# Optimization experiments

Hardware: AMD Instinct MI355X
Metric: run time of the kernel (lower is better)

## Reference

```python
import jax, jax.numpy as jnp
import numpy as np

N, E, NF, EF = 2048, 65536, 128, 64
HID, NH, HD, FF, L = 256, 8, 32, 1024, 4
OUT, MAXN = 1280, 4096


def setup_inputs() -> dict:
    key = jax.random.key(0)
    ks = iter(jax.random.split(key, 64))
    def rn(shape, s=0.02):
        return jax.random.normal(next(ks), shape, jnp.float32) * s
    inp = dict(
        node_features=jax.random.normal(next(ks), (N, NF), jnp.float32),
        edge_features=jax.random.normal(next(ks), (E, EF), jnp.float32),
        edge_index=jax.random.randint(next(ks), (2, E), 0, N),
        W_node=rn((NF, HID)), b_node=jnp.zeros((HID,)),
        W_edge=rn((EF, HID)), b_edge=jnp.zeros((HID,)),
        pos_emb=rn((MAXN, HID), 1.0),
        Wq=rn((L, HID, HID)), bq=jnp.zeros((L, HID)),
        Wk=rn((L, HID, HID)), bk=jnp.zeros((L, HID)),
        Wv=rn((L, HID, HID)), bv=jnp.zeros((L, HID)),
        Wo=rn((L, HID, HID)), bo=jnp.zeros((L, HID)),
        Wep=rn((L, HID, NH)), bep=jnp.zeros((L, NH)),
        Wf1=rn((L, HID, FF)), bf1=jnp.zeros((L, FF)),
        Wf2=rn((L, FF, HID)), bf2=jnp.zeros((L, HID)),
        g1=jnp.ones((L, HID)), be1=jnp.zeros((L, HID)),
        g2=jnp.ones((L, HID)), be2=jnp.zeros((L, HID)),
        g_ln=jnp.ones((HID,)), b_ln=jnp.zeros((HID,)),
        Wp1=rn((HID, HID)), bp1=jnp.zeros((HID,)),
        Wp2=rn((HID, 1)), bp2=jnp.zeros((1,)),
        Wo1=rn((3 * HID, 2 * HID)), bo1=jnp.zeros((2 * HID,)),
        Wo2=rn((2 * HID, OUT)), bo2=jnp.zeros((OUT,)),
    )
    return inp


def _ln(x, g, b, eps=1e-5):
    m = x.mean(-1, keepdims=True)
    v = ((x - m) ** 2).mean(-1, keepdims=True)
    return (x - m) * jax.lax.rsqrt(v + eps) * g + b


def reference(node_features, edge_features, edge_index, W_node, b_node, W_edge,
              b_edge, pos_emb, Wq, bq, Wk, bk, Wv, bv, Wo, bo, Wep, bep,
              Wf1, bf1, Wf2, bf2, g1, be1, g2, be2, g_ln, b_ln,
              Wp1, bp1, Wp2, bp2, Wo1, bo1, Wo2, bo2):
    n = node_features.shape[0]
    src, dst = edge_index[0], edge_index[1]
    scale = float(np.sqrt(HD))
    # node encoding + learned positional embedding (n <= max_nodes path)
    x = node_features @ W_node + b_node + pos_emb[:n]
    edge_attr = edge_features @ W_edge + b_edge  # [E, HID]
    # symmetric adjacency mask with self-loops
    adj = jnp.zeros((n, n), bool).at[src, dst].set(True).at[dst, src].set(True)
    adj = adj.at[jnp.arange(n), jnp.arange(n)].set(True)
    for i in range(L):
        Q = (x @ Wq[i] + bq[i]).reshape(n, NH, HD)
        K = (x @ Wk[i] + bk[i]).reshape(n, NH, HD)
        V = (x @ Wv[i] + bv[i]).reshape(n, NH, HD)
        scores = jnp.einsum('nhd,mhd->nmh', Q, K) / scale  # [n, n, NH]
        ebias = edge_attr @ Wep[i] + bep[i]  # [E, NH]
        scores = scores.at[src, dst].add(ebias)  # accumulating scatter, same as per-edge loop
        scores = jnp.where(adj[:, None, :], scores.transpose(0, 2, 1), -jnp.inf)  # [n, NH, n]
        attn = jax.nn.softmax(scores, axis=-1)
        ctx = jnp.einsum('nhm,mhd->nhd', attn, V).reshape(n, HID)
        a = ctx @ Wo[i] + bo[i]
        x = _ln(x + a, g1[i], be1[i])
        f = jax.nn.gelu(x @ Wf1[i] + bf1[i], approximate=False) @ Wf2[i] + bf2[i]
        x = _ln(x + f, g2[i], be2[i])
    x = _ln(x, g_ln, b_ln)
    # global pooling (batch=None path): mean / max / attention
    mean_p = x.mean(0, keepdims=True)
    max_p = x.max(0, keepdims=True)
    aw = jax.nn.softmax(jnp.tanh(x @ Wp1 + bp1) @ Wp2 + bp2, axis=0)  # [n, 1]
    attn_p = (x * aw).sum(0, keepdims=True)
    g = jnp.concatenate([mean_p, max_p, attn_p], axis=1)  # [1, 3*HID]
    out = jax.nn.relu(g @ Wo1 + bo1) @ Wo2 + bo2  # [1, OUT]
    return out
```

## Files before the change

### kernel.cpp

```cpp
#include <hip/hip_runtime.h>
#include <math.h>

#define NNODE 2048
#define NEDGE 65536
#define HIDN  256
#define NHEAD 8
#define HDIM  32
#define FFD   1024
#define NLAYER 4
#define OUTD  1280
#define NNZ_MAX (2*NEDGE + NNODE)

typedef __attribute__((ext_vector_type(8))) short bf16x8;
typedef __attribute__((ext_vector_type(4))) float f32x4;

__device__ __forceinline__ unsigned short f2b(float f) {
    unsigned u = __float_as_uint(f);
    unsigned r = (u + 0x7fffu + ((u >> 16) & 1u)) >> 16;
    return (unsigned short)r;
}
__device__ __forceinline__ float b2f(unsigned short u) {
    return __uint_as_float((unsigned)u << 16);
}

template<int EPI, int OUT>
__global__ __launch_bounds__(256)
void mgemm(const unsigned short* __restrict__ A, const unsigned short* __restrict__ Bt,
           const float* __restrict__ bias, const float* __restrict__ extra,
           float* __restrict__ Cf, unsigned short* __restrict__ Cb,
           int M, int N, int K)
{
    __shared__ __align__(16) unsigned short As[64 * 40];
    __shared__ __align__(16) unsigned short Bs[64 * 40];
    int tid = threadIdx.x;
    int bm0 = blockIdx.y * 64, bn0 = blockIdx.x * 64;
    int wave = tid >> 6, lane = tid & 63;
    int wm = (wave >> 1) * 32, wn = (wave & 1) * 32;
    int srow = tid >> 2, skoff = (tid & 3) * 8;
    int lrow = lane & 15, quad = lane >> 4;
    f32x4 acc[2][2] = {};
    for (int k0 = 0; k0 < K; k0 += 32) {
        *(uint4*)(&As[srow*40 + skoff]) = *(const uint4*)(A  + (size_t)(bm0+srow)*K + k0 + skoff);
        *(uint4*)(&Bs[srow*40 + skoff]) = *(const uint4*)(Bt + (size_t)(bn0+srow)*K + k0 + skoff);
        __syncthreads();
        bf16x8 af[2], bfr[2];
        #pragma unroll
        for (int i = 0; i < 2; i++) af[i]  = *(const bf16x8*)(&As[(wm + i*16 + lrow)*40 + quad*8]);
        #pragma unroll
        for (int j = 0; j < 2; j++) bfr[j] = *(const bf16x8*)(&Bs[(wn + j*16 + lrow)*40 + quad*8]);
        #pragma unroll
        for (int i = 0; i < 2; i++)
            #pragma unroll
            for (int j = 0; j < 2; j++)
                acc[i][j] = __builtin_amdgcn_mfma_f32_16x16x32_bf16(af[i], bfr[j], acc[i][j], 0, 0, 0);
        __syncthreads();
    }
    #pragma unroll
    for (int i = 0; i < 2; i++)
        #pragma unroll
        for (int j = 0; j < 2; j++) {
            int col = bn0 + wn + j*16 + lrow;
            float bv = bias[col];
            #pragma unroll
            for (int r = 0; r < 4; r++) {
                int row = bm0 + wm + i*16 + quad*4 + r;
                float v = acc[i][j][r] + bv;
                if (EPI == 1) v = 0.5f * v * (1.f + erff(v * 0.70710678118654752f));
                else if (EPI == 2) v = tanhf(v);
                else if (EPI == 3) v += extra[(size_t)row*N + col];
                if (OUT == 0 || OUT == 2) Cf[(size_t)row*N + col] = v;
                if (OUT == 1 || OUT == 2) Cb[(size_t)row*N + col] = f2b(v);
            }
        }
}

__global__ __launch_bounds__(256)
void transpose_bf16(const float* __restrict__ src, unsigned short* __restrict__ dst,
                    int K, int N, long srcStride, long dstStride)
{
    __shared__ unsigned short tile[32][33];
    const float* s = src + (size_t)blockIdx.z * srcStride;
    unsigned short* d = dst + (size_t)blockIdx.z * dstStride;
    int n0 = blockIdx.x * 32, k0 = blockIdx.y * 32;
    int tx = threadIdx.x & 31, ty = threadIdx.x >> 5;
    #pragma unroll
    for (int i = 0; i < 4; i++)
        tile[ty + i*8][tx] = f2b(s[(size_t)(k0 + ty + i*8) * N + n0 + tx]);
    __syncthreads();
    #pragma unroll
    for (int i = 0; i < 4; i++)
        d[(size_t)(n0 + ty + i*8) * K + k0 + tx] = tile[tx][ty + i*8];
}

__global__ void conv_bf16(const float* __restrict__ s, unsigned short* __restrict__ d, int n)
{
    int t = blockIdx.x * 256 + threadIdx.x;
    if (t < n) d[t] = f2b(s[t]);
}

__global__ void concat_qkv_bias(const float* __restrict__ bq, const float* __restrict__ bk,
                                const float* __restrict__ bv, float* __restrict__ bqkv)
{
    int t = blockIdx.x * 256 + threadIdx.x;
    if (t >= NLAYER * 768) return;
    int l = t / 768, j = t % 768;
    float v = (j < 256) ? bq[l*256 + j] : (j < 512 ? bk[l*256 + j - 256] : bv[l*256 + j - 512]);
    bqkv[t] = v;
}

__global__ void adj_build(const int* __restrict__ src, const int* __restrict__ dst,
                          unsigned* __restrict__ adjbits)
{
    int t = blockIdx.x * blockDim.x + threadIdx.x;
    if (t < NEDGE) {
        int s = src[t], d = dst[t];
        atomicOr(&adjbits[(size_t)s*64 + (d >> 5)], 1u << (d & 31));
        atomicOr(&adjbits[(size_t)d*64 + (s >> 5)], 1u << (s & 31));
    }
    if (t < NNODE)
        atomicOr(&adjbits[(size_t)t*64 + (t >> 5)], 1u << (t & 31));
}

__global__ void row_rank(const unsigned* __restrict__ adjbits,
                         unsigned* __restrict__ rowcum, int* __restrict__ deg)
{
    int i = blockIdx.x * blockDim.x + threadIdx.x;
    if (i >= NNODE) return;
    unsigned c = 0;
    for (int w = 0; w < 64; w++) {
        rowcum[i*64 + w] = c;
        c += __popc(adjbits[i*64 + w]);
    }
    deg[i] = (int)c;
}

__global__ __launch_bounds__(256)
void scan_kernel(const int* __restrict__ deg, int* __restrict__ rowoff)
{
    __shared__ int part[256];
    int tid = threadIdx.x;
    int base = tid * 8;
    int local[8]; int s = 0;
    #pragma unroll
    for (int k = 0; k < 8; k++) { local[k] = s; s += deg[base + k]; }
    part[tid] = s;
    __syncthreads();
    for (int off = 1; off < 256; off <<= 1) {
        int v = (tid >= off) ? part[tid - off] : 0;
        __syncthreads();
        part[tid] += v;
        __syncthreads();
    }
    int pre = (tid == 0) ? 0 : part[tid - 1];
    #pragma unroll
    for (int k = 0; k < 8; k++) rowoff[base + k] = pre + local[k];
    if (tid == 255) rowoff[NNODE] = part[255];
}

__global__ void fill_cols(const unsigned* __restrict__ adjbits,
                          const int* __restrict__ rowoff, int* __restrict__ cols)
{
    int i = blockIdx.x * blockDim.x + threadIdx.x;
    if (i >= NNODE) return;
    int base = rowoff[i];
    for (int w = 0; w < 64; w++) {
        unsigned bits = adjbits[i*64 + w];
        while (bits) {
            int b = __ffs(bits) - 1;
            cols[base++] = w*32 + b;
            bits &= bits - 1;
        }
    }
}

__global__ void wcomb_kernel(const float* __restrict__ W_edge, const float* __restrict__ b_edge,
                             const float* __restrict__ Wep, const float* __restrict__ bep,
                             float* __restrict__ Wcomb, float* __restrict__ bcomb)
{
    int t = blockIdx.x * blockDim.x + threadIdx.x;
    if (t < 64*32) {
        int k = t >> 5, lh = t & 31, l = lh >> 3, h = lh & 7;
        float acc = 0.f;
        for (int c = 0; c < HIDN; c++)
            acc += W_edge[k*HIDN + c] * Wep[l*HIDN*NHEAD + c*NHEAD + h];
        Wcomb[k*32 + lh] = acc;
    } else if (t < 64*32 + 32) {
        int lh = t - 64*32, l = lh >> 3, h = lh & 7;
        float acc = bep[l*NHEAD + h];
        for (int c = 0; c < HIDN; c++)
            acc += b_edge[c] * Wep[l*HIDN*NHEAD + c*NHEAD + h];
        bcomb[lh] = acc;
    }
}

__global__ __launch_bounds__(256)
void ebias_kernel(const float* __restrict__ ef, const float* __restrict__ Wcomb,
                  const float* __restrict__ bcomb, float* __restrict__ out)
{
    __shared__ float Wl[64*32];
    __shared__ float bl[32];
    int tid = threadIdx.x;
    for (int k = tid; k < 64*32; k += 256) Wl[k] = Wcomb[k];
    if (tid < 32) bl[tid] = bcomb[tid];
    __syncthreads();
    int t = blockIdx.x * 256 + tid;
    int e = t >> 5, lh = t & 31;
    const float* f = ef + (size_t)e * 64;
    float acc = bl[lh];
    #pragma unroll
    for (int k = 0; k < 64; k++) acc += f[k] * Wl[k*32 + lh];
    out[(size_t)e*32 + lh] = acc;
}

__global__ void scatter_bias(const int* __restrict__ src, const int* __restrict__ dst,
                             const unsigned* __restrict__ adjbits,
                             const unsigned* __restrict__ rowcum,
                             const int* __restrict__ rowoff,
                             const float* __restrict__ ebias, float* __restrict__ bias_csr)
{
    int t = blockIdx.x * blockDim.x + threadIdx.x;
    int e = t >> 5;
    if (e >= NEDGE) return;
    int lh = t & 31;
    int s = src[e], d = dst[e];
    unsigned wbits = adjbits[(size_t)s*64 + (d >> 5)];
    int rank = (int)rowcum[(size_t)s*64 + (d >> 5)] + __popc(wbits & ((1u << (d & 31)) - 1u));
    int slot = rowoff[s] + rank;
    atomicAdd(&bias_csr[(size_t)slot*32 + lh], ebias[(size_t)e*32 + lh]);
}

__global__ __launch_bounds__(256)
void attn_kernel(const unsigned short* __restrict__ QKVb, const int* __restrict__ rowoff,
                 const int* __restrict__ cols, const float* __restrict__ bias_csr,
                 unsigned short* __restrict__ ctxb, int layer)
{
    __shared__ float mS[4][8], lS[4][8];
    __shared__ __align__(16) float accS[4][256];
    int i = blockIdx.x;
    int tid = threadIdx.x;
    int w = tid >> 6, lane = tid & 63;
    int h = lane >> 3;
    int off = lane * 4;
    ushort4 qu = *(const ushort4*)(QKVb + (size_t)i*768 + off);
    float4 qf = { b2f(qu.x), b2f(qu.y), b2f(qu.z), b2f(qu.w) };
    int start = rowoff[i], end = rowoff[i+1];
    int lh0 = layer * 8 + h;
    float m = -INFINITY, l = 0.f;
    float4 acc = {0.f, 0.f, 0.f, 0.f};
    for (int c0 = start + w; c0 < end; c0 += 256) {
        int myslot = c0 + 4*lane;
        int mycol = (myslot < end) ? cols[myslot] : 0;
        int lim = min(end, c0 + 256);
        int it = 0;
        for (int slot = c0; slot < lim; slot += 4, ++it) {
            int j = __shfl(mycol, it);
            ushort4 ku = *(const ushort4*)(QKVb + (size_t)j*768 + 256 + off);
            float s = qf.x*b2f(ku.x) + qf.y*b2f(ku.y) + qf.z*b2f(ku.z) + qf.w*b2f(ku.w);
            s += __shfl_xor(s, 1);
            s += __shfl_xor(s, 2);
            s += __shfl_xor(s, 4);
            s = s * 0.17677669529663687f + bias_csr[(size_t)slot*32 + lh0];
            float mn = fmaxf(m, s);
            float sc = __expf(m - mn);
            float p  = __expf(s - mn);
            ushort4 vu = *(const ushort4*)(QKVb + (size_t)j*768 + 512 + off);
            acc.x = acc.x*sc + p*b2f(vu.x);
            acc.y = acc.y*sc + p*b2f(vu.y);
            acc.z = acc.z*sc + p*b2f(vu.z);
            acc.w = acc.w*sc + p*b2f(vu.w);
            l = l*sc + p;
            m = mn;
        }
    }
    if ((lane & 7) == 0) { mS[w][h] = m; lS[w][h] = l; }
    *(float4*)&accS[w][off] = acc;
    __syncthreads();
    if (w == 0) {
        float m0 = mS[0][h], m1 = mS[1][h], m2 = mS[2][h], m3 = mS[3][h];
        float mx = fmaxf(fmaxf(m0, m1), fmaxf(m2, m3));
        float e0 = (m0 == -INFINITY) ? 0.f : __expf(m0 - mx);
        float e1 = (m1 == -INFINITY) ? 0.f : __expf(m1 - mx);
        float e2 = (m2 == -INFINITY) ? 0.f : __expf(m2 - mx);
        float e3 = (m3 == -INFINITY) ? 0.f : __expf(m3 - mx);
        float ls = lS[0][h]*e0 + lS[1][h]*e1 + lS[2][h]*e2 + lS[3][h]*e3;
        float4 a0 = *(float4*)&accS[0][off];
        float4 a1 = *(float4*)&accS[1][off];
        float4 a2 = *(float4*)&accS[2][off];
        float4 a3 = *(float4*)&accS[3][off];
        float inv = 1.f / ls;
        ushort4 o;
        o.x = f2b((a0.x*e0 + a1.x*e1 + a2.x*e2 + a3.x*e3) * inv);
        o.y = f2b((a0.y*e0 + a1.y*e1 + a2.y*e2 + a3.y*e3) * inv);
        o.z = f2b((a0.z*e0 + a1.z*e1 + a2.z*e2 + a3.z*e3) * inv);
        o.w = f2b((a0.w*e0 + a1.w*e1 + a2.w*e2 + a3.w*e3) * inv);
        *(ushort4*)(ctxb + (size_t)i*HIDN + off) = o;
    }
}

template<bool RES>
__global__ __launch_bounds__(256)
void ln_kernel(float* __restrict__ x, const float* __restrict__ r,
               const float* __restrict__ g, const float* __restrict__ b,
               unsigned short* __restrict__ xb)
{
    __shared__ float lds[4];
    int row = blockIdx.x, c = threadIdx.x;
    float v = x[(size_t)row*HIDN + c];
    if (RES) v += r[(size_t)row*HIDN + c];
    float s = v;
    for (int mm = 1; mm < 64; mm <<= 1) s += __shfl_xor(s, mm);
    if ((c & 63) == 0) lds[c >> 6] = s;
    __syncthreads();
    float mean = (lds[0] + lds[1] + lds[2] + lds[3]) * (1.f / HIDN);
    __syncthreads();
    float dv = v - mean;
    float qq = dv * dv;
    for (int mm = 1; mm < 64; mm <<= 1) qq += __shfl_xor(qq, mm);
    if ((c & 63) == 0) lds[c >> 6] = qq;
    __syncthreads();
    float var = (lds[0] + lds[1] + lds[2] + lds[3]) * (1.f / HIDN);
    float rs = rsqrtf(var + 1e-5f);
    float o = dv * rs * g[c] + b[c];
    x[(size_t)row*HIDN + c] = o;
    xb[(size_t)row*HIDN + c] = f2b(o);
}

__global__ void pool_score(const float* __restrict__ t, const float* __restrict__ Wp2,
                           const float* __restrict__ bp2, float* __restrict__ s)
{
    int i = blockIdx.x * blockDim.x + threadIdx.x;
    if (i >= NNODE) return;
    float acc = bp2[0];
    for (int c = 0; c < HIDN; c++) acc += t[(size_t)i*HIDN + c] * Wp2[c];
    s[i] = acc;
}

__global__ __launch_bounds__(1024)
void softmax_nodes(const float* __restrict__ s, float* __restrict__ aw)
{
    __shared__ float lds[16];
    __shared__ float red;
    int tid = threadIdx.x;
    float a = s[tid], b = s[tid + 1024];
    float mx = fmaxf(a, b);
    for (int mm = 1; mm < 64; mm <<= 1) mx = fmaxf(mx, __shfl_xor(mx, mm));
    if ((tid & 63) == 0) lds[tid >> 6] = mx;
    __syncthreads();
    if (tid == 0) { float v = -INFINITY; for (int k = 0; k < 16; k++) v = fmaxf(v, lds[k]); red = v; }
    __syncthreads();
    mx = red;
    float ea = __expf(a - mx), eb = __expf(b - mx);
    float ss = ea + eb;
    for (int mm = 1; mm < 64; mm <<= 1) ss += __shfl_xor(ss, mm);
    __syncthreads();
    if ((tid & 63) == 0) lds[tid >> 6] = ss;
    __syncthreads();
    if (tid == 0) { float v = 0.f; for (int k = 0; k < 16; k++) v += lds[k]; red = v; }
    __syncthreads();
    ss = red;
    aw[tid] = ea / ss;
    aw[tid + 1024] = eb / ss;
}

__global__ __launch_bounds__(256)
void pool_kernel(const float* __restrict__ x, const float* __restrict__ aw,
                 float* __restrict__ g)
{
    __shared__ float l1[4], l2[4], l3[4];
    int c = blockIdx.x, tid = threadIdx.x;
    float sm = 0.f, mx = -INFINITY, ap = 0.f;
    for (int r = tid; r < NNODE; r += 256) {
        float v = x[(size_t)r*HIDN + c];
        sm += v;
        mx = fmaxf(mx, v);
        ap += v * aw[r];
    }
    for (int mm = 1; mm < 64; mm <<= 1) {
        sm += __shfl_xor(sm, mm);
        mx = fmaxf(mx, __shfl_xor(mx, mm));
        ap += __shfl_xor(ap, mm);
    }
    if ((tid & 63) == 0) { int w = tid >> 6; l1[w] = sm; l2[w] = mx; l3[w] = ap; }
    __syncthreads();
    if (tid == 0) {
        sm = l1[0] + l1[1] + l1[2] + l1[3];
        mx = fmaxf(fmaxf(l2[0], l2[1]), fmaxf(l2[2], l2[3]));
        ap = l3[0] + l3[1] + l3[2] + l3[3];
        g[c]          = sm * (1.f / NNODE);
        g[HIDN + c]   = mx;
        g[2*HIDN + c] = ap;
    }
}

__global__ __launch_bounds__(512)
void head1(const float* __restrict__ g, const float* __restrict__ Wo1,
           const float* __restrict__ bo1, float* __restrict__ h1)
{
    __shared__ float gs[3*HIDN];
    int tid = threadIdx.x;
    for (int k = tid; k < 3*HIDN; k += 512) gs[k] = g[k];
    __syncthreads();
    float acc = bo1[tid];
    for (int k = 0; k < 3*HIDN; k++) acc += gs[k] * Wo1[(size_t)k*512 + tid];
    h1[tid] = fmaxf(acc, 0.f);
}

__global__ __launch_bounds__(256)
void head2(const float* __restrict__ h1, const float* __restrict__ Wo2,
           const float* __restrict__ bo2, float* __restrict__ out)
{
    __shared__ float hs[512];
    int tid = threadIdx.x;
    int j = blockIdx.x * 256 + tid;
    for (int k = tid; k < 512; k += 256) hs[k] = h1[k];
    __syncthreads();
    float acc = bo2[j];
    for (int k = 0; k < 512; k++) acc += hs[k] * Wo2[(size_t)k*OUTD + j];
    out[j] = acc;
}

extern "C" void kernel_launch(void* const* d_in, const int* in_sizes, int n_in,
                              void* d_out, int out_size, void* d_ws, size_t ws_size,
                              hipStream_t stream)
{
    const float* node_features = (const float*)d_in[0];
    const float* edge_features = (const float*)d_in[1];
    const int*   edge_index    = (const int*)d_in[2];
    const float* W_node = (const float*)d_in[3];
    const float* b_node = (const float*)d_in[4];
    const float* W_edge = (const float*)d_in[5];
    const float* b_edge = (const float*)d_in[6];
    const float* pos_emb = (const float*)d_in[7];
    const float* Wq = (const float*)d_in[8];
    const float* bq = (const float*)d_in[9];
    const float* Wk = (const float*)d_in[10];
    const float* bk = (const float*)d_in[11];
    const float* Wv = (const float*)d_in[12];
    const float* bv = (const float*)d_in[13];
    const float* Wo = (const float*)d_in[14];
    const float* bo = (const float*)d_in[15];
    const float* Wep = (const float*)d_in[16];
    const float* bep = (const float*)d_in[17];
    const float* Wf1 = (const float*)d_in[18];
    const float* bf1 = (const float*)d_in[19];
    const float* Wf2 = (const float*)d_in[20];
    const float* bf2 = (const float*)d_in[21];
    const float* g1  = (const float*)d_in[22];
    const float* be1 = (const float*)d_in[23];
    const float* g2  = (const float*)d_in[24];
    const float* be2 = (const float*)d_in[25];
    const float* g_ln = (const float*)d_in[26];
    const float* b_ln = (const float*)d_in[27];
    const float* Wp1 = (const float*)d_in[28];
    const float* bp1 = (const float*)d_in[29];
    const float* Wp2 = (const float*)d_in[30];
    const float* bp2 = (const float*)d_in[31];
    const float* Wo1 = (const float*)d_in[32];
    const float* bo1 = (const float*)d_in[33];
    const float* Wo2 = (const float*)d_in[34];
    const float* bo2 = (const float*)d_in[35];
    const int* src = edge_index;
    const int* dst = edge_index + NEDGE;

    char* w = (char*)d_ws;
    auto carve = [&](size_t nbytes) {
        void* p = (void*)w;
        w += (nbytes + 255) & ~(size_t)255;
        return p;
    };
    float* x        = (float*)carve((size_t)NNODE*HIDN*4);
    unsigned short* xb = (unsigned short*)carve((size_t)NNODE*HIDN*2);
    unsigned short* bufQKVb = (unsigned short*)carve((size_t)NNODE*768*2);
    float* bufO     = (float*)carve((size_t)NNODE*HIDN*4);
    float* bufP     = (float*)carve((size_t)NNODE*HIDN*4);
    unsigned short* bufAb = (unsigned short*)carve((size_t)NNODE*HIDN*2);
    void*  scratchA = carve((size_t)NEDGE*32*4);
    float* bufE     = (float*)scratchA;
    unsigned short* bufFb = (unsigned short*)scratchA;
    float* Wcomb    = (float*)carve(64*32*4);
    float* bcomb    = (float*)carve(32*4);
    unsigned* adjbits = (unsigned*)carve((size_t)NNODE*64*4);
    unsigned* rowcum  = (unsigned*)carve((size_t)NNODE*64*4);
    int* deg    = (int*)carve(NNODE*4);
    int* rowoff = (int*)carve((NNODE+1)*4);
    int* colsb  = (int*)carve((size_t)NNZ_MAX*4);
    float* bias_csr = (float*)carve((size_t)NNZ_MAX*32*4);
    float* sbuf  = (float*)carve(NNODE*4);
    float* awbuf = (float*)carve(NNODE*4);
    float* gbuf  = (float*)carve(3*HIDN*4);
    float* h1buf = (float*)carve(512*4);
    unsigned short* nf_b  = (unsigned short*)carve((size_t)NNODE*128*2);
    unsigned short* WnT   = (unsigned short*)carve((size_t)HIDN*128*2);
    unsigned short* WqkvT = (unsigned short*)carve((size_t)NLAYER*768*HIDN*2);
    float*          bqkv  = (float*)carve((size_t)NLAYER*768*4);
    unsigned short* WoT   = (unsigned short*)carve((size_t)NLAYER*HIDN*HIDN*2);
    unsigned short* Wf1T  = (unsigned short*)carve((size_t)NLAYER*FFD*HIDN*2);
    unsigned short* Wf2T  = (unsigned short*)carve((size_t)NLAYER*HIDN*FFD*2);
    unsigned short* Wp1T  = (unsigned short*)carve((size_t)HIDN*HIDN*2);

    hipMemsetAsync(adjbits, 0, (size_t)NNODE*64*4, stream);
    hipMemsetAsync(bias_csr, 0, (size_t)NNZ_MAX*32*4, stream);
    adj_build<<<(NEDGE+255)/256, 256, 0, stream>>>(src, dst, adjbits);
    row_rank<<<NNODE/256, 256, 0, stream>>>(adjbits, rowcum, deg);
    scan_kernel<<<1, 256, 0, stream>>>(deg, rowoff);
    fill_cols<<<NNODE/256, 256, 0, stream>>>(adjbits, rowoff, colsb);
    wcomb_kernel<<<(64*32+32+255)/256, 256, 0, stream>>>(W_edge, b_edge, Wep, bep, Wcomb, bcomb);
    ebias_kernel<<<(NEDGE*32)/256, 256, 0, stream>>>(edge_features, Wcomb, bcomb, bufE);
    scatter_bias<<<(NEDGE*32)/256, 256, 0, stream>>>(src, dst, adjbits, rowcum, rowoff, bufE, bias_csr);

    conv_bf16<<<(NNODE*128)/256, 256, 0, stream>>>(node_features, nf_b, NNODE*128);
    transpose_bf16<<<dim3(HIDN/32, 128/32, 1), 256, 0, stream>>>(W_node, WnT, 128, HIDN, 0, 0);
    transpose_bf16<<<dim3(8, 8, NLAYER), 256, 0, stream>>>(Wq, WqkvT,            HIDN, HIDN, 65536, 196608);
    transpose_bf16<<<dim3(8, 8, NLAYER), 256, 0, stream>>>(Wk, WqkvT + 65536,    HIDN, HIDN, 65536, 196608);
    transpose_bf16<<<dim3(8, 8, NLAYER), 256, 0, stream>>>(Wv, WqkvT + 131072,   HIDN, HIDN, 65536, 196608);
    transpose_bf16<<<dim3(8, 8, NLAYER), 256, 0, stream>>>(Wo, WoT, HIDN, HIDN, 65536, 65536);
    transpose_bf16<<<dim3(FFD/32, HIDN/32, NLAYER), 256, 0, stream>>>(Wf1, Wf1T, HIDN, FFD, 262144, 262144);
    transpose_bf16<<<dim3(HIDN/32, FFD/32, NLAYER), 256, 0, stream>>>(Wf2, Wf2T, FFD, HIDN, 262144, 262144);
    transpose_bf16<<<dim3(8, 8, 1), 256, 0, stream>>>(Wp1, Wp1T, HIDN, HIDN, 0, 0);
    concat_qkv_bias<<<(NLAYER*768+255)/256, 256, 0, stream>>>(bq, bk, bv, bqkv);

    mgemm<3,2><<<dim3(HIDN/64, NNODE/64), 256, 0, stream>>>(nf_b, WnT, b_node, pos_emb, x, xb, NNODE, HIDN, 128);

    for (int l = 0; l < NLAYER; l++) {
        mgemm<0,1><<<dim3(768/64, NNODE/64), 256, 0, stream>>>(
            xb, WqkvT + (size_t)l*768*HIDN, bqkv + l*768, nullptr, nullptr, bufQKVb, NNODE, 768, HIDN);
        attn_kernel<<<NNODE, 256, 0, stream>>>(bufQKVb, rowoff, colsb, bias_csr, bufAb, l);
        mgemm<0,0><<<dim3(HIDN/64, NNODE/64), 256, 0, stream>>>(
            bufAb, WoT + (size_t)l*HIDN*HIDN, bo + l*HIDN, nullptr, bufO, nullptr, NNODE, HIDN, HIDN);
        ln_kernel<true><<<NNODE, 256, 0, stream>>>(x, bufO, g1 + l*HIDN, be1 + l*HIDN, xb);
        mgemm<1,1><<<dim3(FFD/64, NNODE/64), 256, 0, stream>>>(
            xb, Wf1T + (size_t)l*FFD*HIDN, bf1 + l*FFD, nullptr, nullptr, bufFb, NNODE, FFD, HIDN);
        mgemm<0,0><<<dim3(HIDN/64, NNODE/64), 256, 0, stream>>>(
            bufFb, Wf2T + (size_t)l*HIDN*FFD, bf2 + l*HIDN, nullptr, bufO, nullptr, NNODE, HIDN, FFD);
        ln_kernel<true><<<NNODE, 256, 0, stream>>>(x, bufO, g2 + l*HIDN, be2 + l*HIDN, xb);
    }

    ln_kernel<false><<<NNODE, 256, 0, stream>>>(x, nullptr, g_ln, b_ln, xb);
    mgemm<2,0><<<dim3(HIDN/64, NNODE/64), 256, 0, stream>>>(xb, Wp1T, bp1, nullptr, bufP, nullptr, NNODE, HIDN, HIDN);
    pool_score<<<NNODE/256, 256, 0, stream>>>(bufP, Wp2, bp2, sbuf);
    softmax_nodes<<<1, 1024, 0, stream>>>(sbuf, awbuf);
    pool_kernel<<<HIDN, 256, 0, stream>>>(x, awbuf, gbuf);
    head1<<<1, 512, 0, stream>>>(gbuf, Wo1, bo1, h1buf);
    head2<<<OUTD/256, 256, 0, stream>>>(h1buf, Wo2, bo2, (float*)d_out);
}
```

Measured before the change: 554.9 us.

## Fuse preprocessing and pooling kernels, prefetch GEMM tiles, parallelize CSR column fill

The GEMM now takes K as a template parameter and loads the next K-chunk from global memory into registers while the current tile is in LDS. All weight transposes are merged into one launch, and so are the conversion and bias concat, the edge-bias compute and scatter, and the pooling score, softmax and head kernels. The pooling score uses an atomic row reduction inside the GEMM epilogue and drops bp2, which is valid because softmax is shift-invariant. fill_cols now runs one thread per 32-bit word instead of one per row. Together these remove launch overhead and intermediate buffers, at the cost of atomics, some redundant exp work per pool block and a larger FFN buffer.

```diff
diff --git a/kernel.cpp b/kernel.cpp
--- a/kernel.cpp
+++ b/kernel.cpp
@@ -23,12 +23,12 @@
     return __uint_as_float((unsigned)u << 16);
 }
 
-template<int EPI, int OUT>
+template<int K, int EPI, int OUT>
 __global__ __launch_bounds__(256)
 void mgemm(const unsigned short* __restrict__ A, const unsigned short* __restrict__ Bt,
            const float* __restrict__ bias, const float* __restrict__ extra,
            float* __restrict__ Cf, unsigned short* __restrict__ Cb,
-           int M, int N, int K)
+           int M, int N, const float* __restrict__ Wp2, float* __restrict__ sred)
 {
     __shared__ __align__(16) unsigned short As[64 * 40];
     __shared__ __align__(16) unsigned short Bs[64 * 40];
@@ -38,11 +38,21 @@
     int wm = (wave >> 1) * 32, wn = (wave & 1) * 32;
     int srow = tid >> 2, skoff = (tid & 3) * 8;
     int lrow = lane & 15, quad = lane >> 4;
+    const unsigned short* ap = A  + (size_t)(bm0 + srow) * K + skoff;
+    const unsigned short* bp = Bt + (size_t)(bn0 + srow) * K + skoff;
+    uint4 av = *(const uint4*)ap;
+    uint4 bv = *(const uint4*)bp;
     f32x4 acc[2][2] = {};
-    for (int k0 = 0; k0 < K; k0 += 32) {
-        *(uint4*)(&As[srow*40 + skoff]) = *(const uint4*)(A  + (size_t)(bm0+srow)*K + k0 + skoff);
-        *(uint4*)(&Bs[srow*40 + skoff]) = *(const uint4*)(Bt + (size_t)(bn0+srow)*K + k0 + skoff);
+    constexpr int NC = K / 32;
+    #pragma unroll 8
+    for (int c = 0; c < NC; ++c) {
+        *(uint4*)(&As[srow*40 + skoff]) = av;
+        *(uint4*)(&Bs[srow*40 + skoff]) = bv;
         __syncthreads();
+        if (c + 1 < NC) {
+            av = *(const uint4*)(ap + (c+1)*32);
+            bv = *(const uint4*)(bp + (c+1)*32);
+        }
         bf16x8 af[2], bfr[2];
         #pragma unroll
         for (int i = 0; i < 2; i++) af[i]  = *(const bf16x8*)(&As[(wm + i*16 + lrow)*40 + quad*8]);
@@ -55,16 +65,38 @@
                 acc[i][j] = __builtin_amdgcn_mfma_f32_16x16x32_bf16(af[i], bfr[j], acc[i][j], 0, 0, 0);
         __syncthreads();
     }
+    if (EPI == 4) {
+        #pragma unroll
+        for (int i = 0; i < 2; i++) {
+            #pragma unroll
+            for (int r = 0; r < 4; r++) {
+                int row = bm0 + wm + i*16 + quad*4 + r;
+                float ps = 0.f;
+                #pragma unroll
+                for (int j = 0; j < 2; j++) {
+                    int col = bn0 + wn + j*16 + lrow;
+                    float v = tanhf(acc[i][j][r] + bias[col]);
+                    ps += v * Wp2[col];
+                }
+                ps += __shfl_xor(ps, 1);
+                ps += __shfl_xor(ps, 2);
+                ps += __shfl_xor(ps, 4);
+                ps += __shfl_xor(ps, 8);
+                if (lrow == 0) atomicAdd(&sred[row], ps);
+            }
+        }
+        return;
+    }
     #pragma unroll
     for (int i = 0; i < 2; i++)
         #pragma unroll
         for (int j = 0; j < 2; j++) {
             int col = bn0 + wn + j*16 + lrow;
-            float bv = bias[col];
+            float bvv = bias[col];
             #pragma unroll
             for (int r = 0; r < 4; r++) {
                 int row = bm0 + wm + i*16 + quad*4 + r;
-                float v = acc[i][j][r] + bv;
+                float v = acc[i][j][r] + bvv;
                 if (EPI == 1) v = 0.5f * v * (1.f + erff(v * 0.70710678118654752f));
                 else if (EPI == 2) v = tanhf(v);
                 else if (EPI == 3) v += extra[(size_t)row*N + col];
@@ -75,13 +107,41 @@
 }
 
 __global__ __launch_bounds__(256)
-void transpose_bf16(const float* __restrict__ src, unsigned short* __restrict__ dst,
-                    int K, int N, long srcStride, long dstStride)
+void transpose_all(const float* __restrict__ Wq, const float* __restrict__ Wk,
+                   const float* __restrict__ Wv, const float* __restrict__ Wo,
+                   const float* __restrict__ Wf1, const float* __restrict__ Wf2,
+                   const float* __restrict__ W_node, const float* __restrict__ Wp1,
+                   unsigned short* __restrict__ WqkvT, unsigned short* __restrict__ WoT,
+                   unsigned short* __restrict__ Wf1T, unsigned short* __restrict__ Wf2T,
+                   unsigned short* __restrict__ WnT, unsigned short* __restrict__ Wp1T)
 {
     __shared__ unsigned short tile[32][33];
-    const float* s = src + (size_t)blockIdx.z * srcStride;
-    unsigned short* d = dst + (size_t)blockIdx.z * dstStride;
-    int n0 = blockIdx.x * 32, k0 = blockIdx.y * 32;
+    int bid = blockIdx.x;
+    const float* s; unsigned short* d; int K, N, n0, k0;
+    if (bid < 1024) {
+        int mat = bid >> 6, rem = bid & 63;
+        int m4 = mat & 3, l = mat >> 2;
+        s = (m4 == 0 ? Wq : m4 == 1 ? Wk : m4 == 2 ? Wv : Wo) + (size_t)l * 65536;
+        d = (m4 < 3) ? WqkvT + (size_t)l*196608 + (size_t)m4*65536
+                     : WoT + (size_t)l*65536;
+        K = 256; N = 256; n0 = (rem & 7) * 32; k0 = (rem >> 3) * 32;
+    } else if (bid < 2048) {
+        int idx = bid - 1024; int l = idx >> 8, rem = idx & 255;
+        s = Wf1 + (size_t)l*262144; d = Wf1T + (size_t)l*262144;
+        K = 256; N = 1024; n0 = (rem & 31) * 32; k0 = (rem >> 5) * 32;
+    } else if (bid < 3072) {
+        int idx = bid - 2048; int l = idx >> 8, rem = idx & 255;
+        s = Wf2 + (size_t)l*262144; d = Wf2T + (size_t)l*262144;
+        K = 1024; N = 256; n0 = (rem & 7) * 32; k0 = (rem >> 3) * 32;
+    } else if (bid < 3104) {
+        int rem = bid - 3072;
+        s = W_node; d = WnT;
+        K = 128; N = 256; n0 = (rem & 7) * 32; k0 = (rem >> 3) * 32;
+    } else {
+        int rem = bid - 3104;
+        s = Wp1; d = Wp1T;
+        K = 256; N = 256; n0 = (rem & 7) * 32; k0 = (rem >> 3) * 32;
+    }
     int tx = threadIdx.x & 31, ty = threadIdx.x >> 5;
     #pragma unroll
     for (int i = 0; i < 4; i++)
@@ -92,20 +152,21 @@
         d[(size_t)(n0 + ty + i*8) * K + k0 + tx] = tile[tx][ty + i*8];
 }
 
-__global__ void conv_bf16(const float* __restrict__ s, unsigned short* __restrict__ d, int n)
+__global__ void misc_prep(const float* __restrict__ nf, unsigned short* __restrict__ nf_b,
+                          const float* __restrict__ bq, const float* __restrict__ bk,
+                          const float* __restrict__ bv, float* __restrict__ bqkv)
 {
     int t = blockIdx.x * 256 + threadIdx.x;
-    if (t < n) d[t] = f2b(s[t]);
-}
-
-__global__ void concat_qkv_bias(const float* __restrict__ bq, const float* __restrict__ bk,
-                                const float* __restrict__ bv, float* __restrict__ bqkv)
-{
-    int t = blockIdx.x * 256 + threadIdx.x;
-    if (t >= NLAYER * 768) return;
-    int l = t / 768, j = t % 768;
-    float v = (j < 256) ? bq[l*256 + j] : (j < 512 ? bk[l*256 + j - 256] : bv[l*256 + j - 512]);
-    bqkv[t] = v;
+    if (t < NNODE*128) {
+        nf_b[t] = f2b(nf[t]);
+    } else {
+        int u = t - NNODE*128;
+        if (u < NLAYER*768) {
+            int l = u / 768, j = u % 768;
+            float v = (j < 256) ? bq[l*256 + j] : (j < 512 ? bk[l*256 + j - 256] : bv[l*256 + j - 512]);
+            bqkv[u] = v;
+        }
+    }
 }
 
 __global__ void adj_build(const int* __restrict__ src, const int* __restrict__ dst,
@@ -157,19 +218,18 @@
     if (tid == 255) rowoff[NNODE] = part[255];
 }
 
-__global__ void fill_cols(const unsigned* __restrict__ adjbits,
-                          const int* __restrict__ rowoff, int* __restrict__ cols)
-{
-    int i = blockIdx.x * blockDim.x + threadIdx.x;
-    if (i >= NNODE) return;
-    int base = rowoff[i];
-    for (int w = 0; w < 64; w++) {
-        unsigned bits = adjbits[i*64 + w];
-        while (bits) {
-            int b = __ffs(bits) - 1;
-            cols[base++] = w*32 + b;
-            bits &= bits - 1;
-        }
+__global__ __launch_bounds__(256)
+void fill_cols(const unsigned* __restrict__ adjbits, const int* __restrict__ rowoff,
+               const unsigned* __restrict__ rowcum, int* __restrict__ cols)
+{
+    int t = blockIdx.x * 256 + threadIdx.x;
+    int i = t >> 6, w = t & 63;
+    unsigned bits = adjbits[(size_t)i*64 + w];
+    int base = rowoff[i] + (int)rowcum[(size_t)i*64 + w];
+    while (bits) {
+        int b = __ffs(bits) - 1;
+        cols[base++] = w*32 + b;
+        bits &= bits - 1;
     }
 }
 
@@ -194,8 +254,12 @@
 }
 
 __global__ __launch_bounds__(256)
-void ebias_kernel(const float* __restrict__ ef, const float* __restrict__ Wcomb,
-                  const float* __restrict__ bcomb, float* __restrict__ out)
+void edge_bias_scatter(const float* __restrict__ ef, const float* __restrict__ Wcomb,
+                       const float* __restrict__ bcomb,
+                       const int* __restrict__ src, const int* __restrict__ dst,
+                       const unsigned* __restrict__ adjbits,
+                       const unsigned* __restrict__ rowcum,
+                       const int* __restrict__ rowoff, float* __restrict__ bias_csr)
 {
     __shared__ float Wl[64*32];
     __shared__ float bl[32];
@@ -209,24 +273,11 @@
     float acc = bl[lh];
     #pragma unroll
     for (int k = 0; k < 64; k++) acc += f[k] * Wl[k*32 + lh];
-    out[(size_t)e*32 + lh] = acc;
-}
-
-__global__ void scatter_bias(const int* __restrict__ src, const int* __restrict__ dst,
-                             const unsigned* __restrict__ adjbits,
-                             const unsigned* __restrict__ rowcum,
-                             const int* __restrict__ rowoff,
-                             const float* __restrict__ ebias, float* __restrict__ bias_csr)
-{
-    int t = blockIdx.x * blockDim.x + threadIdx.x;
-    int e = t >> 5;
-    if (e >= NEDGE) return;
-    int lh = t & 31;
     int s = src[e], d = dst[e];
     unsigned wbits = adjbits[(size_t)s*64 + (d >> 5)];
     int rank = (int)rowcum[(size_t)s*64 + (d >> 5)] + __popc(wbits & ((1u << (d & 31)) - 1u));
     int slot = rowoff[s] + rank;
-    atomicAdd(&bias_csr[(size_t)slot*32 + lh], ebias[(size_t)e*32 + lh]);
+    atomicAdd(&bias_csr[(size_t)slot*32 + lh], acc);
 }
 
 __global__ __launch_bounds__(256)
@@ -325,55 +376,38 @@
     xb[(size_t)row*HIDN + c] = f2b(o);
 }
 
-__global__ void pool_score(const float* __restrict__ t, const float* __restrict__ Wp2,
-                           const float* __restrict__ bp2, float* __restrict__ s)
-{
-    int i = blockIdx.x * blockDim.x + threadIdx.x;
-    if (i >= NNODE) return;
-    float acc = bp2[0];
-    for (int c = 0; c < HIDN; c++) acc += t[(size_t)i*HIDN + c] * Wp2[c];
-    s[i] = acc;
-}
-
-__global__ __launch_bounds__(1024)
-void softmax_nodes(const float* __restrict__ s, float* __restrict__ aw)
-{
-    __shared__ float lds[16];
-    __shared__ float red;
-    int tid = threadIdx.x;
-    float a = s[tid], b = s[tid + 1024];
-    float mx = fmaxf(a, b);
-    for (int mm = 1; mm < 64; mm <<= 1) mx = fmaxf(mx, __shfl_xor(mx, mm));
-    if ((tid & 63) == 0) lds[tid >> 6] = mx;
-    __syncthreads();
-    if (tid == 0) { float v = -INFINITY; for (int k = 0; k < 16; k++) v = fmaxf(v, lds[k]); red = v; }
-    __syncthreads();
-    mx = red;
-    float ea = __expf(a - mx), eb = __expf(b - mx);
-    float ss = ea + eb;
-    for (int mm = 1; mm < 64; mm <<= 1) ss += __shfl_xor(ss, mm);
-    __syncthreads();
-    if ((tid & 63) == 0) lds[tid >> 6] = ss;
-    __syncthreads();
-    if (tid == 0) { float v = 0.f; for (int k = 0; k < 16; k++) v += lds[k]; red = v; }
-    __syncthreads();
-    ss = red;
-    aw[tid] = ea / ss;
-    aw[tid + 1024] = eb / ss;
-}
-
-__global__ __launch_bounds__(256)
-void pool_kernel(const float* __restrict__ x, const float* __restrict__ aw,
-                 float* __restrict__ g)
-{
+__global__ __launch_bounds__(256)
+void pool_fused(const float* __restrict__ x, const float* __restrict__ sred,
+                float* __restrict__ g)
+{
+    __shared__ float sl[NNODE];
+    __shared__ float red[4];
     __shared__ float l1[4], l2[4], l3[4];
     int c = blockIdx.x, tid = threadIdx.x;
+    float mxs = -INFINITY;
+    for (int r = tid; r < NNODE; r += 256) {
+        float v = sred[r];
+        sl[r] = v;
+        mxs = fmaxf(mxs, v);
+    }
+    for (int mm = 1; mm < 64; mm <<= 1) mxs = fmaxf(mxs, __shfl_xor(mxs, mm));
+    if ((tid & 63) == 0) red[tid >> 6] = mxs;
+    __syncthreads();
+    mxs = fmaxf(fmaxf(red[0], red[1]), fmaxf(red[2], red[3]));
+    __syncthreads();
+    float ss = 0.f;
+    for (int r = tid; r < NNODE; r += 256) ss += __expf(sl[r] - mxs);
+    for (int mm = 1; mm < 64; mm <<= 1) ss += __shfl_xor(ss, mm);
+    if ((tid & 63) == 0) red[tid >> 6] = ss;
+    __syncthreads();
+    ss = red[0] + red[1] + red[2] + red[3];
+    float inv = 1.f / ss;
     float sm = 0.f, mx = -INFINITY, ap = 0.f;
     for (int r = tid; r < NNODE; r += 256) {
         float v = x[(size_t)r*HIDN + c];
         sm += v;
         mx = fmaxf(mx, v);
-        ap += v * aw[r];
+        ap += v * __expf(sl[r] - mxs) * inv;
     }
     for (int mm = 1; mm < 64; mm <<= 1) {
         sm += __shfl_xor(sm, mm);
@@ -393,30 +427,24 @@
 }
 
 __global__ __launch_bounds__(512)
-void head1(const float* __restrict__ g, const float* __restrict__ Wo1,
-           const float* __restrict__ bo1, float* __restrict__ h1)
+void head_fused(const float* __restrict__ g, const float* __restrict__ Wo1,
+                const float* __restrict__ bo1, const float* __restrict__ Wo2,
+                const float* __restrict__ bo2, float* __restrict__ out)
 {
     __shared__ float gs[3*HIDN];
+    __shared__ float hs[512];
     int tid = threadIdx.x;
     for (int k = tid; k < 3*HIDN; k += 512) gs[k] = g[k];
     __syncthreads();
     float acc = bo1[tid];
     for (int k = 0; k < 3*HIDN; k++) acc += gs[k] * Wo1[(size_t)k*512 + tid];
-    h1[tid] = fmaxf(acc, 0.f);
-}
-
-__global__ __launch_bounds__(256)
-void head2(const float* __restrict__ h1, const float* __restrict__ Wo2,
-           const float* __restrict__ bo2, float* __restrict__ out)
-{
-    __shared__ float hs[512];
-    int tid = threadIdx.x;
-    int j = blockIdx.x * 256 + tid;
-    for (int k = tid; k < 512; k += 256) hs[k] = h1[k];
-    __syncthreads();
-    float acc = bo2[j];
-    for (int k = 0; k < 512; k++) acc += hs[k] * Wo2[(size_t)k*OUTD + j];
-    out[j] = acc;
+    hs[tid] = fmaxf(acc, 0.f);
+    __syncthreads();
+    for (int j = tid; j < OUTD; j += 512) {
+        float a2 = bo2[j];
+        for (int k = 0; k < 512; k++) a2 += hs[k] * Wo2[(size_t)k*OUTD + j];
+        out[j] = a2;
+    }
 }
 
 extern "C" void kernel_launch(void* const* d_in, const int* in_sizes, int n_in,
@@ -459,6 +487,7 @@
     const float* bo1 = (const float*)d_in[33];
     const float* Wo2 = (const float*)d_in[34];
     const float* bo2 = (const float*)d_in[35];
+    (void)bp2;
     const int* src = edge_index;
     const int* dst = edge_index + NEDGE;
 
@@ -472,23 +501,18 @@
     unsigned short* xb = (unsigned short*)carve((size_t)NNODE*HIDN*2);
     unsigned short* bufQKVb = (unsigned short*)carve((size_t)NNODE*768*2);
     float* bufO     = (float*)carve((size_t)NNODE*HIDN*4);
-    float* bufP     = (float*)carve((size_t)NNODE*HIDN*4);
     unsigned short* bufAb = (unsigned short*)carve((size_t)NNODE*HIDN*2);
-    void*  scratchA = carve((size_t)NEDGE*32*4);
-    float* bufE     = (float*)scratchA;
-    unsigned short* bufFb = (unsigned short*)scratchA;
+    unsigned short* bufFb = (unsigned short*)carve((size_t)NNODE*FFD*2);
     float* Wcomb    = (float*)carve(64*32*4);
     float* bcomb    = (float*)carve(32*4);
     unsigned* adjbits = (unsigned*)carve((size_t)NNODE*64*4);
+    float* bias_csr = (float*)carve((size_t)NNZ_MAX*32*4);
+    float* sbuf  = (float*)carve(NNODE*4);
     unsigned* rowcum  = (unsigned*)carve((size_t)NNODE*64*4);
     int* deg    = (int*)carve(NNODE*4);
     int* rowoff = (int*)carve((NNODE+1)*4);
     int* colsb  = (int*)carve((size_t)NNZ_MAX*4);
-    float* bias_csr = (float*)carve((size_t)NNZ_MAX*32*4);
-    float* sbuf  = (float*)carve(NNODE*4);
-    float* awbuf = (float*)carve(NNODE*4);
     float* gbuf  = (float*)carve(3*HIDN*4);
-    float* h1buf = (float*)carve(512*4);
     unsigned short* nf_b  = (unsigned short*)carve((size_t)NNODE*128*2);
     unsigned short* WnT   = (unsigned short*)carve((size_t)HIDN*128*2);
     unsigned short* WqkvT = (unsigned short*)carve((size_t)NLAYER*768*HIDN*2);
@@ -498,48 +522,41 @@
     unsigned short* Wf2T  = (unsigned short*)carve((size_t)NLAYER*HIDN*FFD*2);
     unsigned short* Wp1T  = (unsigned short*)carve((size_t)HIDN*HIDN*2);
 
-    hipMemsetAsync(adjbits, 0, (size_t)NNODE*64*4, stream);
-    hipMemsetAsync(bias_csr, 0, (size_t)NNZ_MAX*32*4, stream);
+    hipMemsetAsync(adjbits, 0,
+                   (size_t)NNODE*64*4 + (size_t)NNZ_MAX*32*4 + (size_t)NNODE*4, stream);
     adj_build<<<(NEDGE+255)/256, 256, 0, stream>>>(src, dst, adjbits);
     row_rank<<<NNODE/256, 256, 0, stream>>>(adjbits, rowcum, deg);
     scan_kernel<<<1, 256, 0, stream>>>(deg, rowoff);
-    fill_cols<<<NNODE/256, 256, 0, stream>>>(adjbits, rowoff, colsb);
+    fill_cols<<<(NNODE*64)/256, 256, 0, stream>>>(adjbits, rowoff, rowcum, colsb);
     wcomb_kernel<<<(64*32+32+255)/256, 256, 0, stream>>>(W_edge, b_edge, Wep, bep, Wcomb, bcomb);
-    ebias_kernel<<<(NEDGE*32)/256, 256, 0, stream>>>(edge_features, Wcomb, bcomb, bufE);
-    scatter_bias<<<(NEDGE*32)/256, 256, 0, stream>>>(src, dst, adjbits, rowcum, rowoff, bufE, bias_csr);
-
-    conv_bf16<<<(NNODE*128)/256, 256, 0, stream>>>(node_features, nf_b, NNODE*128);
-    transpose_bf16<<<dim3(HIDN/32, 128/32, 1), 256, 0, stream>>>(W_node, WnT, 128, HIDN, 0, 0);
-    transpose_bf16<<<dim3(8, 8, NLAYER), 256, 0, stream>>>(Wq, WqkvT,            HIDN, HIDN, 65536, 196608);
-    transpose_bf16<<<dim3(8, 8, NLAYER), 256, 0, stream>>>(Wk, WqkvT + 65536,    HIDN, HIDN, 65536, 196608);
-    transpose_bf16<<<dim3(8, 8, NLAYER), 256, 0, stream>>>(Wv, WqkvT + 131072,   HIDN, HIDN, 65536, 196608);
-    transpose_bf16<<<dim3(8, 8, NLAYER), 256, 0, stream>>>(Wo, WoT, HIDN, HIDN, 65536, 65536);
-    transpose_bf16<<<dim3(FFD/32, HIDN/32, NLAYER), 256, 0, stream>>>(Wf1, Wf1T, HIDN, FFD, 262144, 262144);
-    transpose_bf16<<<dim3(HIDN/32, FFD/32, NLAYER), 256, 0, stream>>>(Wf2, Wf2T, FFD, HIDN, 262144, 262144);
-    transpose_bf16<<<dim3(8, 8, 1), 256, 0, stream>>>(Wp1, Wp1T, HIDN, HIDN, 0, 0);
-    concat_qkv_bias<<<(NLAYER*768+255)/256, 256, 0, stream>>>(bq, bk, bv, bqkv);
-
-    mgemm<3,2><<<dim3(HIDN/64, NNODE/64), 256, 0, stream>>>(nf_b, WnT, b_node, pos_emb, x, xb, NNODE, HIDN, 128);
+    edge_bias_scatter<<<(NEDGE*32)/256, 256, 0, stream>>>(
+        edge_features, Wcomb, bcomb, src, dst, adjbits, rowcum, rowoff, bias_csr);
+
+    misc_prep<<<(NNODE*128 + NLAYER*768 + 255)/256, 256, 0, stream>>>(
+        node_features, nf_b, bq, bk, bv, bqkv);
+    transpose_all<<<3168, 256, 0, stream>>>(Wq, Wk, Wv, Wo, Wf1, Wf2, W_node, Wp1,
+                                            WqkvT, WoT, Wf1T, Wf2T, WnT, Wp1T);
+
+    mgemm<128,3,2><<<dim3(HIDN/64, NNODE/64), 256, 0, stream>>>(
+        nf_b, WnT, b_node, pos_emb, x, xb, NNODE, HIDN, nullptr, nullptr);
 
     for (int l = 0; l < NLAYER; l++) {
-        mgemm<0,1><<<dim3(768/64, NNODE/64), 256, 0, stream>>>(
-            xb, WqkvT + (size_t)l*768*HIDN, bqkv + l*768, nullptr, nullptr, bufQKVb, NNODE, 768, HIDN);
+        mgemm<256,0,1><<<dim3(768/64, NNODE/64), 256, 0, stream>>>(
+            xb, WqkvT + (size_t)l*768*HIDN, bqkv + l*768, nullptr, nullptr, bufQKVb, NNODE, 768, nullptr, nullptr);
         attn_kernel<<<NNODE, 256, 0, stream>>>(bufQKVb, rowoff, colsb, bias_csr, bufAb, l);
-        mgemm<0,0><<<dim3(HIDN/64, NNODE/64), 256, 0, stream>>>(
-            bufAb, WoT + (size_t)l*HIDN*HIDN, bo + l*HIDN, nullptr, bufO, nullptr, NNODE, HIDN, HIDN);
+        mgemm<256,0,0><<<dim3(HIDN/64, NNODE/64), 256, 0, stream>>>(
+            bufAb, WoT + (size_t)l*HIDN*HIDN, bo + l*HIDN, nullptr, bufO, nullptr, NNODE, HIDN, nullptr, nullptr);
         ln_kernel<true><<<NNODE, 256, 0, stream>>>(x, bufO, g1 + l*HIDN, be1 + l*HIDN, xb);
-        mgemm<1,1><<<dim3(FFD/64, NNODE/64), 256, 0, stream>>>(
-            xb, Wf1T + (size_t)l*FFD*HIDN, bf1 + l*FFD, nullptr, nullptr, bufFb, NNODE, FFD, HIDN);
-        mgemm<0,0><<<dim3(HIDN/64, NNODE/64), 256, 0, stream>>>(
-            bufFb, Wf2T + (size_t)l*HIDN*FFD, bf2 + l*HIDN, nullptr, bufO, nullptr, NNODE, HIDN, FFD);
+        mgemm<256,1,1><<<dim3(FFD/64, NNODE/64), 256, 0, stream>>>(
+            xb, Wf1T + (size_t)l*FFD*HIDN, bf1 + l*FFD, nullptr, nullptr, bufFb, NNODE, FFD, nullptr, nullptr);
+        mgemm<1024,0,0><<<dim3(HIDN/64, NNODE/64), 256, 0, stream>>>(
+            bufFb, Wf2T + (size_t)l*HIDN*FFD, bf2 + l*HIDN, nullptr, bufO, nullptr, NNODE, HIDN, nullptr, nullptr);
         ln_kernel<true><<<NNODE, 256, 0, stream>>>(x, bufO, g2 + l*HIDN, be2 + l*HIDN, xb);
     }
 
     ln_kernel<false><<<NNODE, 256, 0, stream>>>(x, nullptr, g_ln, b_ln, xb);
-    mgemm<2,0><<<dim3(HIDN/64, NNODE/64), 256, 0, stream>>>(xb, Wp1T, bp1, nullptr, bufP, nullptr, NNODE, HIDN, HIDN);
-    pool_score<<<NNODE/256, 256, 0, stream>>>(bufP, Wp2, bp2, sbuf);
-    softmax_nodes<<<1, 1024, 0, stream>>>(sbuf, awbuf);
-    pool_kernel<<<HIDN, 256, 0, stream>>>(x, awbuf, gbuf);
-    head1<<<1, 512, 0, stream>>>(gbuf, Wo1, bo1, h1buf);
-    head2<<<OUTD/256, 256, 0, stream>>>(h1buf, Wo2, bo2, (float*)d_out);
-}
+    mgemm<256,4,0><<<dim3(HIDN/64, NNODE/64), 256, 0, stream>>>(
+        xb, Wp1T, bp1, nullptr, nullptr, nullptr, NNODE, HIDN, Wp2, sbuf);
+    pool_fused<<<HIDN, 256, 0, stream>>>(x, sbuf, gbuf);
+    head_fused<<<1, 512, 0, stream>>>(gbuf, Wo1, bo1, Wo2, bo2, (float*)d_out);
+}
```

Measured after the change: 500.7 us. -9.8%, faster.
